# Kernel tuning notes

Measured on AMD Instinct MI355X. Metric: run time of the kernel, lower is better.

## Reference

```python
import jax, jax.numpy as jnp
import numpy as np


def setup_inputs() -> dict:
    key = jax.random.key(0)
    ks = jax.random.split(key, 8)
    B, N, D, E, S = 8, 4096, 1024, 64, 2
    H = D
    T = E * S  # total slots = 128
    return {
        "x": jax.random.normal(ks[0], (B, N, D), jnp.float32),
        "phi_w": jax.random.normal(ks[1], (T, D), jnp.float32) * 0.02,
        "fc1_w": jax.random.normal(ks[2], (E, H, D), jnp.float32) * 0.02,
        "fc1_b": jax.random.normal(ks[3], (E, H), jnp.float32) * 0.02,
        "fc2_w": jax.random.normal(ks[4], (E, D, H), jnp.float32) * 0.02,
        "fc2_b": jax.random.normal(ks[5], (E, D), jnp.float32) * 0.02,
        "out_w": jax.random.normal(ks[6], (D, D), jnp.float32) * 0.02,
        "out_b": jax.random.normal(ks[7], (D,), jnp.float32) * 0.02,
    }


def reference(x, phi_w, fc1_w, fc1_b, fc2_w, fc2_b, out_w, out_b):
    B, N, D = x.shape
    E, H, _ = fc1_w.shape
    T = phi_w.shape[0]
    S = T // E
    # dispatch logits: (B, N, T)
    logits = jnp.einsum('bnd,td->bnt', x, phi_w)
    dispatch_w = jax.nn.softmax(logits, axis=1)  # softmax over tokens
    combine_w = jax.nn.softmax(logits, axis=2)   # softmax over slots
    # dispatch: compress tokens -> slots, (B, T, D) -> (B, E, S, D)
    slots = jnp.einsum('bnt,bnd->btd', dispatch_w, x).reshape(B, E, S, D)
    # per-expert tiny MLP (no weight duplication over B)
    h = jnp.einsum('besd,ehd->besh', slots, fc1_w) + fc1_b[None, :, None, :]
    h = jax.nn.gelu(h, approximate=True)  # tanh approximation, matches torch
    out = jnp.einsum('besh,edh->besd', h, fc2_w) + fc2_b[None, :, None, :]
    out = out.reshape(B, T, D)
    # combine: expand slots -> tokens
    combined = jnp.einsum('bnt,btd->bnd', combine_w, out)
    output = jnp.einsum('bnd,od->bno', combined, out_w) + out_b
    aux_loss = jnp.asarray(0.0, dtype=x.dtype)
    return output, aux_loss
```

## Files before the change

kernel.cpp:

```cpp
#include <hip/hip_runtime.h>
#include <math.h>

#define B_ 8
#define N_ 4096
#define D_ 1024
#define E_ 64
#define T_ 128

using bf16   = __bf16;
using bf16x4 = __attribute__((ext_vector_type(4))) __bf16;
using bf16x8 = __attribute__((ext_vector_type(8))) __bf16;
using f32x4  = __attribute__((ext_vector_type(4))) float;

#define MFMA16(a, b, c) __builtin_amdgcn_mfma_f32_16x16x32_bf16(a, b, c, 0, 0, 0)
#define LDK 72

__device__ __forceinline__ bf16x8 ldsfrag(const bf16* p) {
  const int lane = threadIdx.x & 63;
  return *(const bf16x8*)(p + (lane & 15) * LDK + (lane >> 4) * 8);
}

__device__ __forceinline__ bf16x8 cvt8(float4 a, float4 b) {
  return (bf16x8){(bf16)a.x, (bf16)a.y, (bf16)a.z, (bf16)a.w,
                  (bf16)b.x, (bf16)b.y, (bf16)b.z, (bf16)b.w};
}

__global__ void k_convert(const float* __restrict__ phi, const float* __restrict__ ow,
                          bf16* __restrict__ phi_bf, bf16* __restrict__ ow_bf)
{
  if (blockIdx.x < 128) {
    int i = blockIdx.x * 256 + threadIdx.x;
    float4 v = ((const float4*)phi)[i];
    ((bf16x4*)phi_bf)[i] = (bf16x4){(bf16)v.x, (bf16)v.y, (bf16)v.z, (bf16)v.w};
  } else {
    int i = (blockIdx.x - 128) * 256 + threadIdx.x;
    float4 v = ((const float4*)ow)[i];
    ((bf16x4*)ow_bf)[i] = (bf16x4){(bf16)v.x, (bf16)v.y, (bf16)v.z, (bf16)v.w};
  }
}

__global__ __launch_bounds__(256) void k_logits(
    const float* __restrict__ X, const bf16* __restrict__ Phi,
    float* __restrict__ L, bf16* __restrict__ Xbf, bf16* __restrict__ CW,
    float* __restrict__ redM, float* __restrict__ redS)
{
  __shared__ __align__(16) char smraw[34048];
  bf16 (*As)[LDK] = (bf16(*)[LDK])smraw;
  bf16 (*Bs)[LDK] = (bf16(*)[LDK])(smraw + 64 * LDK * 2);
  float (*S)[133] = (float(*)[133])smraw;

  const int m0 = blockIdx.x * 64;
  const int tid = threadIdx.x;
  const int wave = tid >> 6, lane = tid & 63;
  const int wm = (wave >> 1) * 32;
  const int wn = (wave & 1) * 64;

  f32x4 acc[2][4];
#pragma unroll
  for (int i = 0; i < 2; ++i)
#pragma unroll
    for (int j = 0; j < 4; ++j) acc[i][j] = (f32x4){0.f, 0.f, 0.f, 0.f};

  const int ar = tid >> 2, ac = (tid & 3) * 16;
  const int br = tid >> 1, bc = (tid & 1) * 32;

  for (int k0 = 0; k0 < 1024; k0 += 64) {
    const float* xp = X + (long)(m0 + ar) * 1024 + k0 + ac;
    float4 v0 = *(const float4*)(xp + 0);
    float4 v1 = *(const float4*)(xp + 4);
    float4 v2 = *(const float4*)(xp + 8);
    float4 v3 = *(const float4*)(xp + 12);
    bf16x8 p0 = cvt8(v0, v1);
    bf16x8 p1 = cvt8(v2, v3);
    *(bf16x8*)&As[ar][ac]     = p0;
    *(bf16x8*)&As[ar][ac + 8] = p1;
    bf16* xo = Xbf + (long)(m0 + ar) * 1024 + k0 + ac;
    *(bf16x8*)xo       = p0;
    *(bf16x8*)(xo + 8) = p1;

    const bf16* pp = Phi + (long)br * 1024 + k0 + bc;
    *(bf16x8*)&Bs[br][bc + 0]  = *(const bf16x8*)(pp + 0);
    *(bf16x8*)&Bs[br][bc + 8]  = *(const bf16x8*)(pp + 8);
    *(bf16x8*)&Bs[br][bc + 16] = *(const bf16x8*)(pp + 16);
    *(bf16x8*)&Bs[br][bc + 24] = *(const bf16x8*)(pp + 24);
    __syncthreads();
#pragma unroll
    for (int kk = 0; kk < 64; kk += 32) {
      bf16x8 a0 = ldsfrag(&As[wm][kk]);
      bf16x8 a1 = ldsfrag(&As[wm + 16][kk]);
#pragma unroll
      for (int n = 0; n < 4; ++n) {
        bf16x8 bb = ldsfrag(&Bs[wn + n * 16][kk]);
        acc[0][n] = MFMA16(a0, bb, acc[0][n]);
        acc[1][n] = MFMA16(a1, bb, acc[1][n]);
      }
    }
    __syncthreads();
  }
  const int cc = lane & 15, rr = (lane >> 4) * 4;
#pragma unroll
  for (int m = 0; m < 2; ++m)
#pragma unroll
    for (int n = 0; n < 4; ++n)
#pragma unroll
      for (int j = 0; j < 4; ++j) {
        const float val = acc[m][n][j];
        L[(long)(m0 + wm + m * 16 + rr + j) * 128 + wn + n * 16 + cc] = val;
        S[wm + m * 16 + rr + j][wn + n * 16 + cc] = val;
      }
  __syncthreads();

  const int r = tid >> 2, q = tid & 3;
  float v[32];
#pragma unroll
  for (int i = 0; i < 8; ++i)
#pragma unroll
    for (int j = 0; j < 4; ++j) v[i * 4 + j] = S[r][q * 4 + i * 16 + j];
  float mx = -1e30f;
#pragma unroll
  for (int i = 0; i < 32; ++i) mx = fmaxf(mx, v[i]);
  mx = fmaxf(mx, __shfl_xor(mx, 1));
  mx = fmaxf(mx, __shfl_xor(mx, 2));
  float sum = 0.f;
#pragma unroll
  for (int i = 0; i < 32; ++i) { v[i] = expf(v[i] - mx); sum += v[i]; }
  sum += __shfl_xor(sum, 1);
  sum += __shfl_xor(sum, 2);
  const float inv = 1.f / sum;
  bf16* cwr = CW + (long)(m0 + r) * 128 + q * 4;
#pragma unroll
  for (int i = 0; i < 8; ++i)
    *(bf16x4*)(cwr + i * 16) = (bf16x4){(bf16)(v[i*4+0]*inv), (bf16)(v[i*4+1]*inv),
                                        (bf16)(v[i*4+2]*inv), (bf16)(v[i*4+3]*inv)};

  if (tid < 128) {
    const int t = tid;
    float m = -1e30f, s = 0.f;
    for (int rj = 0; rj < 64; ++rj) {
      float val = S[rj][t];
      if (val > m) { s = s * expf(m - val) + 1.f; m = val; }
      else         { s += expf(val - m); }
    }
    const long chunk = m0 >> 6;
    redM[chunk * 128 + t] = m;
    redS[chunk * 128 + t] = s;
  }
}

__global__ void disp_final(const float* __restrict__ redM, const float* __restrict__ redS,
                           float* __restrict__ Mf, float* __restrict__ Zf)
{
  int idx = blockIdx.x * 256 + threadIdx.x;
  int b = idx >> 7, t = idx & 127;
  float m = -1e30f, s = 0.f;
  for (int c = 0; c < 64; ++c) {
    float mc = redM[((long)b * 64 + c) * 128 + t];
    float sc = redS[((long)b * 64 + c) * 128 + t];
    float nm = fmaxf(m, mc);
    s = s * expf(m - nm) + sc * expf(mc - nm);
    m = nm;
  }
  Mf[idx] = m;
  Zf[idx] = 1.f / s;
}

__global__ __launch_bounds__(256) void k_dwt(const float* __restrict__ L,
    const float* __restrict__ Mf, const float* __restrict__ Zf, bf16* __restrict__ DWT)
{
  __shared__ float S[64][132];
  const int b = blockIdx.y, n0 = blockIdx.x * 64;
  const int tid = threadIdx.x;
  const int r = tid >> 2;
  const int c0 = (tid & 3) * 32;
  const float* Lp = L + ((long)b * N_ + n0 + r) * T_ + c0;
#pragma unroll
  for (int i = 0; i < 32; i += 4) {
    float4 v = *(const float4*)(Lp + i);
    S[r][c0 + i + 0] = v.x;
    S[r][c0 + i + 1] = v.y;
    S[r][c0 + i + 2] = v.z;
    S[r][c0 + i + 3] = v.w;
  }
  __syncthreads();
  const int nc = (tid & 7) * 8;
  for (int ti = tid >> 3; ti < 128; ti += 32) {
    const float mf = Mf[b * 128 + ti], zf = Zf[b * 128 + ti];
    bf16x8 o;
#pragma unroll
    for (int j = 0; j < 8; ++j) o[j] = (bf16)(expf(S[nc + j][ti] - mf) * zf);
    *(bf16x8*)(DWT + ((long)b * 128 + ti) * 4096 + n0 + nc) = o;
  }
}

__device__ __forceinline__ bf16x8 ldsfragB(const bf16 (*Bs)[LDK], int dbase, int kk) {
  const int l = threadIdx.x & 63;
  const int d = dbase + (l & 15);
  const int c = ((l >> 4) * 8 + kk) ^ (((d >> 5) & 3) << 4);
  return *(const bf16x8*)(&Bs[d][c]);
}

__global__ __launch_bounds__(256) void k_slots(
    const bf16* __restrict__ DWT, const bf16* __restrict__ Xbf, bf16* __restrict__ Part)
{
  __shared__ bf16 As[128][LDK];
  __shared__ bf16 Bs[128][LDK];
  const int b = blockIdx.z >> 3, chunk = blockIdx.z & 7;
  const int d0 = blockIdx.x * 128;
  const int tid = threadIdx.x, wave = tid >> 6, lane = tid & 63;
  const int wm = (wave >> 1) * 64, wn = (wave & 1) * 64;

  f32x4 acc[4][4];
#pragma unroll
  for (int i = 0; i < 4; ++i)
#pragma unroll
    for (int j = 0; j < 4; ++j) acc[i][j] = (f32x4){0.f, 0.f, 0.f, 0.f};

  const int at = tid >> 1, anc = (tid & 1) * 32;
  const int bn = tid >> 2, bq = tid & 3, bdc = bq * 32;
  const int bcol = bn ^ (bq << 4);
  const long dwt_b = (long)b * 128 * 4096;
  const long x_b   = (long)b * 4096 * 1024;

  for (int k0 = 0; k0 < 512; k0 += 64) {
    const int nbase = chunk * 512 + k0;
    const bf16* ap = DWT + dwt_b + (long)at * 4096 + nbase + anc;
    *(bf16x8*)&As[at][anc + 0]  = *(const bf16x8*)(ap + 0);
    *(bf16x8*)&As[at][anc + 8]  = *(const bf16x8*)(ap + 8);
    *(bf16x8*)&As[at][anc + 16] = *(const bf16x8*)(ap + 16);
    *(bf16x8*)&As[at][anc + 24] = *(const bf16x8*)(ap + 24);
    const bf16* xp = Xbf + x_b + (long)(nbase + bn) * 1024 + d0 + bdc;
    bf16x8 q0 = *(const bf16x8*)(xp + 0);
    bf16x8 q1 = *(const bf16x8*)(xp + 8);
    bf16x8 q2 = *(const bf16x8*)(xp + 16);
    bf16x8 q3 = *(const bf16x8*)(xp + 24);
#pragma unroll
    for (int i = 0; i < 8; ++i) {
      Bs[bdc + i][bcol]      = q0[i];
      Bs[bdc + 8 + i][bcol]  = q1[i];
      Bs[bdc + 16 + i][bcol] = q2[i];
      Bs[bdc + 24 + i][bcol] = q3[i];
    }
    __syncthreads();
#pragma unroll
    for (int kk = 0; kk < 64; kk += 32) {
      bf16x8 af[4], bfr[4];
#pragma unroll
      for (int m = 0; m < 4; ++m) af[m]  = ldsfrag(&As[wm + m * 16][kk]);
#pragma unroll
      for (int n = 0; n < 4; ++n) bfr[n] = ldsfragB(Bs, wn + n * 16, kk);
#pragma unroll
      for (int m = 0; m < 4; ++m)
#pragma unroll
        for (int n = 0; n < 4; ++n)
          acc[m][n] = MFMA16(af[m], bfr[n], acc[m][n]);
    }
    __syncthreads();
  }
  const int cc = lane & 15, rr = (lane >> 4) * 4;
  bf16* Cp = Part + ((long)chunk * 8 + b) * 128 * 1024;
#pragma unroll
  for (int m = 0; m < 4; ++m)
#pragma unroll
    for (int n = 0; n < 4; ++n)
#pragma unroll
      for (int j = 0; j < 4; ++j)
        Cp[(long)(wm + m * 16 + rr + j) * 1024 + d0 + wn + n * 16 + cc] =
            (bf16)acc[m][n][j];
}

__global__ void k_reduce8(const bf16* __restrict__ P, bf16* __restrict__ O)
{
  long base = ((long)blockIdx.x * 256 + threadIdx.x) * 8;
  f32x4 slo = (f32x4){0.f,0.f,0.f,0.f}, shi = (f32x4){0.f,0.f,0.f,0.f};
#pragma unroll
  for (int c = 0; c < 8; ++c) {
    bf16x8 v = *(const bf16x8*)(P + (long)c * 1048576 + base);
#pragma unroll
    for (int j = 0; j < 4; ++j) { slo[j] += (float)v[j]; shi[j] += (float)v[4 + j]; }
  }
  bf16x8 o;
#pragma unroll
  for (int j = 0; j < 4; ++j) { o[j] = (bf16)slo[j]; o[4 + j] = (bf16)shi[j]; }
  *(bf16x8*)(O + base) = o;
}

template<int GELU, int INL>
__global__ __launch_bounds__(256) void k_expert(
    const bf16* __restrict__ Ab, const float* __restrict__ W,
    const float* __restrict__ bias, bf16* __restrict__ Out)
{
  __shared__ bf16 As[16][LDK];
  __shared__ bf16 Bs[64][LDK];
  const int e = blockIdx.y;
  const int h0 = blockIdx.x * 64;
  const int tid = threadIdx.x, wave = tid >> 6, lane = tid & 63;
  f32x4 acc = (f32x4){0.f, 0.f, 0.f, 0.f};

  const int hr = tid >> 2, kc = (tid & 3) * 16;

  for (int k0 = 0; k0 < 1024; k0 += 64) {
    if (tid < 128) {
      int r = tid >> 3, akc = (tid & 7) * 8;
      long row = (INL == 0) ? (long)((r >> 1) * 128 + e * 2 + (r & 1)) : (long)(e * 16 + r);
      *(bf16x8*)&As[r][akc] = *(const bf16x8*)(Ab + row * 1024 + k0 + akc);
    }
    const float* wp = W + ((long)e * 1024 + h0 + hr) * 1024 + k0 + kc;
    float4 w0 = *(const float4*)(wp + 0);
    float4 w1 = *(const float4*)(wp + 4);
    float4 w2 = *(const float4*)(wp + 8);
    float4 w3 = *(const float4*)(wp + 12);
    *(bf16x8*)&Bs[hr][kc]     = cvt8(w0, w1);
    *(bf16x8*)&Bs[hr][kc + 8] = cvt8(w2, w3);
    __syncthreads();
    bf16x8 a0 = ldsfrag(&As[0][0]);
    bf16x8 b0 = ldsfrag(&Bs[wave * 16][0]);
    acc = MFMA16(a0, b0, acc);
    a0 = ldsfrag(&As[0][32]);
    b0 = ldsfrag(&Bs[wave * 16][32]);
    acc = MFMA16(a0, b0, acc);
    __syncthreads();
  }
  const int cc = lane & 15, rr = (lane >> 4) * 4;
  const int h = h0 + wave * 16 + cc;
  const float bs = bias[e * 1024 + h];
#pragma unroll
  for (int j = 0; j < 4; ++j) {
    float v = acc[j] + bs;
    if (GELU) {
      float x3 = v * v * v;
      v = 0.5f * v * (1.f + tanhf(0.7978845608028654f * (v + 0.044715f * x3)));
    }
    int m = rr + j;
    long orow = (INL == 0) ? (long)(e * 16 + m) : (long)((m >> 1) * 128 + e * 2 + (m & 1));
    Out[orow * 1024 + h] = (bf16)v;
  }
}

__global__ __launch_bounds__(256) void k_proj(
    const bf16* __restrict__ OWbf, const bf16* __restrict__ OS, bf16* __restrict__ PT)
{
  __shared__ bf16 As[64][LDK];
  __shared__ bf16 Bs[64][LDK];
  const int o0 = blockIdx.y * 64, t0 = blockIdx.x * 64;
  const int tid = threadIdx.x, wave = tid >> 6, lane = tid & 63;
  const int wm = (wave >> 1) * 32, wn = (wave & 1) * 32;
  f32x4 acc[2][2];
#pragma unroll
  for (int i = 0; i < 2; ++i)
#pragma unroll
    for (int j = 0; j < 2; ++j) acc[i][j] = (f32x4){0.f, 0.f, 0.f, 0.f};

  const int r = tid >> 2, kc = (tid & 3) * 16;
  for (int k0 = 0; k0 < 1024; k0 += 64) {
    const bf16* apo = OWbf + (long)(o0 + r) * 1024 + k0 + kc;
    *(bf16x8*)&As[r][kc]     = *(const bf16x8*)(apo + 0);
    *(bf16x8*)&As[r][kc + 8] = *(const bf16x8*)(apo + 8);
    const bf16* bpo = OS + (long)(t0 + r) * 1024 + k0 + kc;
    *(bf16x8*)&Bs[r][kc]     = *(const bf16x8*)(bpo + 0);
    *(bf16x8*)&Bs[r][kc + 8] = *(const bf16x8*)(bpo + 8);
    __syncthreads();
#pragma unroll
    for (int kk = 0; kk < 64; kk += 32) {
      bf16x8 a0 = ldsfrag(&As[wm][kk]);
      bf16x8 a1 = ldsfrag(&As[wm + 16][kk]);
      bf16x8 b0 = ldsfrag(&Bs[wn][kk]);
      bf16x8 b1 = ldsfrag(&Bs[wn + 16][kk]);
      acc[0][0] = MFMA16(a0, b0, acc[0][0]);
      acc[0][1] = MFMA16(a0, b1, acc[0][1]);
      acc[1][0] = MFMA16(a1, b0, acc[1][0]);
      acc[1][1] = MFMA16(a1, b1, acc[1][1]);
    }
    __syncthreads();
  }
  const int cc = lane & 15, rr = (lane >> 4) * 4;
#pragma unroll
  for (int m = 0; m < 2; ++m)
#pragma unroll
    for (int n = 0; n < 2; ++n)
#pragma unroll
      for (int j = 0; j < 4; ++j)
        PT[(long)(o0 + wm + m * 16 + rr + j) * 1024 + t0 + wn + n * 16 + cc] =
            (bf16)acc[m][n][j];
}

__global__ __launch_bounds__(256) void k_combine(
    const bf16* __restrict__ CW, const bf16* __restrict__ PT,
    const float* __restrict__ ob, float* __restrict__ O)
{
  __shared__ bf16 As[128][LDK];
  __shared__ bf16 Bs[128][LDK];
  const int b = blockIdx.z, m0 = blockIdx.y * 128, o0 = blockIdx.x * 128;
  const int tid = threadIdx.x, wave = tid >> 6, lane = tid & 63;
  const int wm = (wave >> 1) * 64, wn = (wave & 1) * 64;

  if (blockIdx.x == 0 && blockIdx.y == 0 && blockIdx.z == 0 && tid == 0)
    O[(long)B_ * N_ * D_] = 0.f;

  f32x4 acc[4][4];
#pragma unroll
  for (int i = 0; i < 4; ++i)
#pragma unroll
    for (int j = 0; j < 4; ++j) acc[i][j] = (f32x4){0.f, 0.f, 0.f, 0.f};

  const int r = tid >> 1, tc = (tid & 1) * 32;
  for (int k0 = 0; k0 < 128; k0 += 64) {
    const bf16* ap = CW + ((long)b * N_ + m0 + r) * 128 + k0 + tc;
    *(bf16x8*)&As[r][tc + 0]  = *(const bf16x8*)(ap + 0);
    *(bf16x8*)&As[r][tc + 8]  = *(const bf16x8*)(ap + 8);
    *(bf16x8*)&As[r][tc + 16] = *(const bf16x8*)(ap + 16);
    *(bf16x8*)&As[r][tc + 24] = *(const bf16x8*)(ap + 24);
    const bf16* bp = PT + (long)(o0 + r) * 1024 + b * 128 + k0 + tc;
    *(bf16x8*)&Bs[r][tc + 0]  = *(const bf16x8*)(bp + 0);
    *(bf16x8*)&Bs[r][tc + 8]  = *(const bf16x8*)(bp + 8);
    *(bf16x8*)&Bs[r][tc + 16] = *(const bf16x8*)(bp + 16);
    *(bf16x8*)&Bs[r][tc + 24] = *(const bf16x8*)(bp + 24);
    __syncthreads();
#pragma unroll
    for (int kk = 0; kk < 64; kk += 32) {
      bf16x8 af[4], bfr[4];
#pragma unroll
      for (int m = 0; m < 4; ++m) af[m]  = ldsfrag(&As[wm + m * 16][kk]);
#pragma unroll
      for (int n = 0; n < 4; ++n) bfr[n] = ldsfrag(&Bs[wn + n * 16][kk]);
#pragma unroll
      for (int m = 0; m < 4; ++m)
#pragma unroll
        for (int n = 0; n < 4; ++n)
          acc[m][n] = MFMA16(af[m], bfr[n], acc[m][n]);
    }
    __syncthreads();
  }
  const int cc = lane & 15, rr = (lane >> 4) * 4;
#pragma unroll
  for (int n = 0; n < 4; ++n) {
    const int o = o0 + wn + n * 16 + cc;
    const float bv = ob[o];
#pragma unroll
    for (int m = 0; m < 4; ++m)
#pragma unroll
      for (int j = 0; j < 4; ++j)
        O[((long)b * N_ + m0 + wm + m * 16 + rr + j) * 1024 + o] = acc[m][n][j] + bv;
  }
}

extern "C" void kernel_launch(void* const* d_in, const int* in_sizes, int n_in,
                              void* d_out, int out_size, void* d_ws, size_t ws_size,
                              hipStream_t stream)
{
  const float* x     = (const float*)d_in[0];
  const float* phi_w = (const float*)d_in[1];
  const float* fc1_w = (const float*)d_in[2];
  const float* fc1_b = (const float*)d_in[3];
  const float* fc2_w = (const float*)d_in[4];
  const float* fc2_b = (const float*)d_in[5];
  const float* out_w = (const float*)d_in[6];
  const float* out_b = (const float*)d_in[7];
  float* out = (float*)d_out;

  float* ws     = (float*)d_ws;
  float* logits = ws;
  float* redM   = logits + 4194304;
  float* redS   = redM + 65536;
  float* Mf     = redS + 65536;
  float* Zf     = Mf + 1024;
  bf16* DWT     = (bf16*)(Zf + 1024);
  bf16* CW      = DWT + 4194304;
  bf16* slots   = CW + 4194304;
  bf16* hbuf    = slots + 1048576;
  bf16* outs    = hbuf + 1048576;
  bf16* projT   = outs + 1048576;
  bf16* phi_bf  = projT + 1048576;
  bf16* outw_bf = phi_bf + 131072;

  bf16* Xbf   = (bf16*)d_out;
  bf16* Part  = Xbf + 33554432;

  k_convert<<<dim3(1152), 256, 0, stream>>>(phi_w, out_w, phi_bf, outw_bf);
  k_logits<<<dim3(512), 256, 0, stream>>>(x, phi_bf, logits, Xbf, CW, redM, redS);
  disp_final<<<dim3(4), 256, 0, stream>>>(redM, redS, Mf, Zf);
  k_dwt<<<dim3(64, 8), 256, 0, stream>>>(logits, Mf, Zf, DWT);
  k_slots<<<dim3(8, 1, 64), 256, 0, stream>>>(DWT, Xbf, Part);
  k_reduce8<<<dim3(512), 256, 0, stream>>>(Part, slots);
  k_expert<1, 0><<<dim3(16, 64), 256, 0, stream>>>(slots, fc1_w, fc1_b, hbuf);
  k_expert<0, 1><<<dim3(16, 64), 256, 0, stream>>>(hbuf, fc2_w, fc2_b, outs);
  k_proj<<<dim3(16, 16), 256, 0, stream>>>(outw_bf, outs, projT);
  k_combine<<<dim3(8, 32, 8), 256, 0, stream>>>(CW, projT, out_b, out);
}
```

Baseline: 321.2 us.

## Drop bf16 copy of x and fold dispatch softmax finalize into k_dwt

k_logits no longer writes a bf16 copy of x. k_slots now reads fp32 x directly and converts it to bf16 while staging into shared memory. The separate disp_final kernel is removed, and each k_dwt block recomputes the per-slot max and normalizer from the partial reductions in shared memory. This cuts a 64 MB write, one kernel launch and a tiny low-occupancy kernel, at the cost of reading fp32 x (twice the bytes) in k_slots and redundant reduction work across the 64 k_dwt blocks per batch.

After: 324.8 us. About the same (+1.1%).

```diff
diff --git a/kernel.cpp b/kernel.cpp
--- a/kernel.cpp
+++ b/kernel.cpp
@@ -41,7 +41,7 @@
 
 __global__ __launch_bounds__(256) void k_logits(
     const float* __restrict__ X, const bf16* __restrict__ Phi,
-    float* __restrict__ L, bf16* __restrict__ Xbf, bf16* __restrict__ CW,
+    float* __restrict__ L, bf16* __restrict__ CW,
     float* __restrict__ redM, float* __restrict__ redS)
 {
   __shared__ __align__(16) char smraw[34048];
@@ -70,13 +70,8 @@
     float4 v1 = *(const float4*)(xp + 4);
     float4 v2 = *(const float4*)(xp + 8);
     float4 v3 = *(const float4*)(xp + 12);
-    bf16x8 p0 = cvt8(v0, v1);
-    bf16x8 p1 = cvt8(v2, v3);
-    *(bf16x8*)&As[ar][ac]     = p0;
-    *(bf16x8*)&As[ar][ac + 8] = p1;
-    bf16* xo = Xbf + (long)(m0 + ar) * 1024 + k0 + ac;
-    *(bf16x8*)xo       = p0;
-    *(bf16x8*)(xo + 8) = p1;
+    *(bf16x8*)&As[ar][ac]     = cvt8(v0, v1);
+    *(bf16x8*)&As[ar][ac + 8] = cvt8(v2, v3);
 
     const bf16* pp = Phi + (long)br * 1024 + k0 + bc;
     *(bf16x8*)&Bs[br][bc + 0]  = *(const bf16x8*)(pp + 0);
@@ -147,27 +142,12 @@
   }
 }
 
-__global__ void disp_final(const float* __restrict__ redM, const float* __restrict__ redS,
-                           float* __restrict__ Mf, float* __restrict__ Zf)
-{
-  int idx = blockIdx.x * 256 + threadIdx.x;
-  int b = idx >> 7, t = idx & 127;
-  float m = -1e30f, s = 0.f;
-  for (int c = 0; c < 64; ++c) {
-    float mc = redM[((long)b * 64 + c) * 128 + t];
-    float sc = redS[((long)b * 64 + c) * 128 + t];
-    float nm = fmaxf(m, mc);
-    s = s * expf(m - nm) + sc * expf(mc - nm);
-    m = nm;
-  }
-  Mf[idx] = m;
-  Zf[idx] = 1.f / s;
-}
-
 __global__ __launch_bounds__(256) void k_dwt(const float* __restrict__ L,
-    const float* __restrict__ Mf, const float* __restrict__ Zf, bf16* __restrict__ DWT)
+    const float* __restrict__ redM, const float* __restrict__ redS,
+    bf16* __restrict__ DWT)
 {
   __shared__ float S[64][132];
+  __shared__ float sMf[128], sZf[128];
   const int b = blockIdx.y, n0 = blockIdx.x * 64;
   const int tid = threadIdx.x;
   const int r = tid >> 2;
@@ -181,10 +161,23 @@
     S[r][c0 + i + 2] = v.z;
     S[r][c0 + i + 3] = v.w;
   }
+  if (tid < 128) {
+    const int t = tid;
+    float m = -1e30f, s = 0.f;
+    for (int c = 0; c < 64; ++c) {
+      float mc = redM[((long)b * 64 + c) * 128 + t];
+      float sc = redS[((long)b * 64 + c) * 128 + t];
+      float nm = fmaxf(m, mc);
+      s = s * expf(m - nm) + sc * expf(mc - nm);
+      m = nm;
+    }
+    sMf[t] = m;
+    sZf[t] = 1.f / s;
+  }
   __syncthreads();
   const int nc = (tid & 7) * 8;
   for (int ti = tid >> 3; ti < 128; ti += 32) {
-    const float mf = Mf[b * 128 + ti], zf = Zf[b * 128 + ti];
+    const float mf = sMf[ti], zf = sZf[ti];
     bf16x8 o;
 #pragma unroll
     for (int j = 0; j < 8; ++j) o[j] = (bf16)(expf(S[nc + j][ti] - mf) * zf);
@@ -200,7 +193,7 @@
 }
 
 __global__ __launch_bounds__(256) void k_slots(
-    const bf16* __restrict__ DWT, const bf16* __restrict__ Xbf, bf16* __restrict__ Part)
+    const bf16* __restrict__ DWT, const float* __restrict__ X, bf16* __restrict__ Part)
 {
   __shared__ bf16 As[128][LDK];
   __shared__ bf16 Bs[128][LDK];
@@ -228,18 +221,13 @@
     *(bf16x8*)&As[at][anc + 8]  = *(const bf16x8*)(ap + 8);
     *(bf16x8*)&As[at][anc + 16] = *(const bf16x8*)(ap + 16);
     *(bf16x8*)&As[at][anc + 24] = *(const bf16x8*)(ap + 24);
-    const bf16* xp = Xbf + x_b + (long)(nbase + bn) * 1024 + d0 + bdc;
-    bf16x8 q0 = *(const bf16x8*)(xp + 0);
-    bf16x8 q1 = *(const bf16x8*)(xp + 8);
-    bf16x8 q2 = *(const bf16x8*)(xp + 16);
-    bf16x8 q3 = *(const bf16x8*)(xp + 24);
-#pragma unroll
-    for (int i = 0; i < 8; ++i) {
-      Bs[bdc + i][bcol]      = q0[i];
-      Bs[bdc + 8 + i][bcol]  = q1[i];
-      Bs[bdc + 16 + i][bcol] = q2[i];
-      Bs[bdc + 24 + i][bcol] = q3[i];
-    }
+    const float* xp = X + x_b + (long)(nbase + bn) * 1024 + d0 + bdc;
+    float fv[32];
+#pragma unroll
+    for (int i = 0; i < 8; ++i)
+      *(float4*)&fv[i * 4] = *(const float4*)(xp + i * 4);
+#pragma unroll
+    for (int i = 0; i < 32; ++i) Bs[bdc + i][bcol] = (bf16)fv[i];
     __syncthreads();
 #pragma unroll
     for (int kk = 0; kk < 64; kk += 32) {
@@ -461,9 +449,7 @@
   float* logits = ws;
   float* redM   = logits + 4194304;
   float* redS   = redM + 65536;
-  float* Mf     = redS + 65536;
-  float* Zf     = Mf + 1024;
-  bf16* DWT     = (bf16*)(Zf + 1024);
+  bf16* DWT     = (bf16*)(redS + 65536);
   bf16* CW      = DWT + 4194304;
   bf16* slots   = CW + 4194304;
   bf16* hbuf    = slots + 1048576;
@@ -472,14 +458,12 @@
   bf16* phi_bf  = projT + 1048576;
   bf16* outw_bf = phi_bf + 131072;
 
-  bf16* Xbf   = (bf16*)d_out;
-  bf16* Part  = Xbf + 33554432;
+  bf16* Part = (bf16*)d_out;
 
   k_convert<<<dim3(1152), 256, 0, stream>>>(phi_w, out_w, phi_bf, outw_bf);
-  k_logits<<<dim3(512), 256, 0, stream>>>(x, phi_bf, logits, Xbf, CW, redM, redS);
-  disp_final<<<dim3(4), 256, 0, stream>>>(redM, redS, Mf, Zf);
-  k_dwt<<<dim3(64, 8), 256, 0, stream>>>(logits, Mf, Zf, DWT);
-  k_slots<<<dim3(8, 1, 64), 256, 0, stream>>>(DWT, Xbf, Part);
+  k_logits<<<dim3(512), 256, 0, stream>>>(x, phi_bf, logits, CW, redM, redS);
+  k_dwt<<<dim3(64, 8), 256, 0, stream>>>(logits, redM, redS, DWT);
+  k_slots<<<dim3(8, 1, 64), 256, 0, stream>>>(DWT, x, Part);
   k_reduce8<<<dim3(512), 256, 0, stream>>>(Part, slots);
   k_expert<1, 0><<<dim3(16, 64), 256, 0, stream>>>(slots, fc1_w, fc1_b, hbuf);
   k_expert<0, 1><<<dim3(16, 64), 256, 0, stream>>>(hbuf, fc2_w, fc2_b, outs);
```

## Stream expert weights directly into MFMA fragments and remap slots grid

Applied to the files above, without the earlier changes.

The expert kernel now stages the full 16x1024 activation tile in LDS once, then each lane loads fp32 weights straight from global memory into registers, converts them to bf16 and feeds the MFMA. This drops the per-k-step LDS staging of weights and the two barriers per iteration. The slots kernel grid is also transposed so batch/chunk index is on x and the D tile on y, which changes block scheduling order. Each lane now reads 32-byte strided rows of the weights, which may coalesce less well than the old tiled loads.

Result: faster. 305.3 us (-5.0%).

```diff
diff --git a/kernel.cpp b/kernel.cpp
--- a/kernel.cpp
+++ b/kernel.cpp
@@ -14,6 +14,7 @@
 
 #define MFMA16(a, b, c) __builtin_amdgcn_mfma_f32_16x16x32_bf16(a, b, c, 0, 0, 0)
 #define LDK 72
+#define LDK3 1032
 
 __device__ __forceinline__ bf16x8 ldsfrag(const bf16* p) {
   const int lane = threadIdx.x & 63;
@@ -204,8 +205,9 @@
 {
   __shared__ bf16 As[128][LDK];
   __shared__ bf16 Bs[128][LDK];
-  const int b = blockIdx.z >> 3, chunk = blockIdx.z & 7;
-  const int d0 = blockIdx.x * 128;
+  const int bz = blockIdx.x;
+  const int b = bz >> 3, chunk = bz & 7;
+  const int d0 = blockIdx.y * 128;
   const int tid = threadIdx.x, wave = tid >> 6, lane = tid & 63;
   const int wm = (wave >> 1) * 64, wn = (wave & 1) * 64;
 
@@ -289,37 +291,35 @@
     const bf16* __restrict__ Ab, const float* __restrict__ W,
     const float* __restrict__ bias, bf16* __restrict__ Out)
 {
-  __shared__ bf16 As[16][LDK];
-  __shared__ bf16 Bs[64][LDK];
+  __shared__ bf16 As[16][LDK3];
   const int e = blockIdx.y;
   const int h0 = blockIdx.x * 64;
   const int tid = threadIdx.x, wave = tid >> 6, lane = tid & 63;
+
+  {
+    const int r = tid >> 4, c = (tid & 15) * 64;
+    const long arow = (INL == 0) ? (long)((r >> 1) * 128 + e * 2 + (r & 1))
+                                 : (long)(e * 16 + r);
+    const bf16* ap = Ab + arow * 1024 + c;
+#pragma unroll
+    for (int i = 0; i < 8; ++i)
+      *(bf16x8*)&As[r][c + i * 8] = *(const bf16x8*)(ap + i * 8);
+  }
+  __syncthreads();
+
   f32x4 acc = (f32x4){0.f, 0.f, 0.f, 0.f};
-
-  const int hr = tid >> 2, kc = (tid & 3) * 16;
-
-  for (int k0 = 0; k0 < 1024; k0 += 64) {
-    if (tid < 128) {
-      int r = tid >> 3, akc = (tid & 7) * 8;
-      long row = (INL == 0) ? (long)((r >> 1) * 128 + e * 2 + (r & 1)) : (long)(e * 16 + r);
-      *(bf16x8*)&As[r][akc] = *(const bf16x8*)(Ab + row * 1024 + k0 + akc);
-    }
-    const float* wp = W + ((long)e * 1024 + h0 + hr) * 1024 + k0 + kc;
-    float4 w0 = *(const float4*)(wp + 0);
-    float4 w1 = *(const float4*)(wp + 4);
-    float4 w2 = *(const float4*)(wp + 8);
-    float4 w3 = *(const float4*)(wp + 12);
-    *(bf16x8*)&Bs[hr][kc]     = cvt8(w0, w1);
-    *(bf16x8*)&Bs[hr][kc + 8] = cvt8(w2, w3);
-    __syncthreads();
-    bf16x8 a0 = ldsfrag(&As[0][0]);
-    bf16x8 b0 = ldsfrag(&Bs[wave * 16][0]);
-    acc = MFMA16(a0, b0, acc);
-    a0 = ldsfrag(&As[0][32]);
-    b0 = ldsfrag(&Bs[wave * 16][32]);
-    acc = MFMA16(a0, b0, acc);
-    __syncthreads();
-  }
+  const float* wbase = W + ((long)e * 1024 + h0 + wave * 16 + (lane & 15)) * 1024
+                         + (lane >> 4) * 8;
+  const bf16* abase = &As[lane & 15][(lane >> 4) * 8];
+#pragma unroll 4
+  for (int k0 = 0; k0 < 1024; k0 += 32) {
+    float4 wa = *(const float4*)(wbase + k0);
+    float4 wb = *(const float4*)(wbase + k0 + 4);
+    bf16x8 bfrag = cvt8(wa, wb);
+    bf16x8 afrag = *(const bf16x8*)(abase + k0);
+    acc = MFMA16(afrag, bfrag, acc);
+  }
+
   const int cc = lane & 15, rr = (lane >> 4) * 4;
   const int h = h0 + wave * 16 + cc;
   const float bs = bias[e * 1024 + h];
@@ -479,7 +479,7 @@
   k_logits<<<dim3(512), 256, 0, stream>>>(x, phi_bf, logits, Xbf, CW, redM, redS);
   disp_final<<<dim3(4), 256, 0, stream>>>(redM, redS, Mf, Zf);
   k_dwt<<<dim3(64, 8), 256, 0, stream>>>(logits, Mf, Zf, DWT);
-  k_slots<<<dim3(8, 1, 64), 256, 0, stream>>>(DWT, Xbf, Part);
+  k_slots<<<dim3(64, 8), 256, 0, stream>>>(DWT, Xbf, Part);
   k_reduce8<<<dim3(512), 256, 0, stream>>>(Part, slots);
   k_expert<1, 0><<<dim3(16, 64), 256, 0, stream>>>(slots, fc1_w, fc1_b, hbuf);
   k_expert<0, 1><<<dim3(16, 64), 256, 0, stream>>>(hbuf, fc2_w, fc2_b, outs);
```
